# Performance work log

Measured on AMD Instinct MI355X. Metric: run time of the kernel, lower is better.

The kernel has to match this reference:

```python
import jax, jax.numpy as jnp
import numpy as np

N = 50000      # nodes
E = 800000     # edges (avg degree 16)
IN_DIM = 256
OUT_DIM = 256
H = 8          # heads
HD = OUT_DIM // H  # head_dim = 32


def setup_inputs() -> dict:
    key = jax.random.key(0)
    k = jax.random.split(key, 6)
    x = jax.random.normal(k[0], (N, IN_DIM), jnp.float32)
    edge_index = jax.random.randint(k[1], (2, E), 0, N, dtype=jnp.int64)
    s = 1.0 / np.sqrt(IN_DIM)
    W_src = jax.random.normal(k[2], (IN_DIM, OUT_DIM), jnp.float32) * s
    W_dst = jax.random.normal(k[3], (IN_DIM, OUT_DIM), jnp.float32) * s
    b_src = jnp.zeros((OUT_DIM,), jnp.float32)
    b_dst = jnp.zeros((OUT_DIM,), jnp.float32)
    # xavier-ish scale for [H, 2*HD] attention vector
    attn_vec = jax.random.normal(k[4], (H, 2 * HD), jnp.float32) * np.sqrt(2.0 / (H + 2 * HD))
    return {"x": x, "edge_index": edge_index, "W_src": W_src, "b_src": b_src,
            "W_dst": W_dst, "b_dst": b_dst, "attn_vec": attn_vec}


def reference(x, edge_index, W_src, b_src, W_dst, b_dst, attn_vec):
    # Linear projections -> [N, H, HD]
    proj_src = (x @ W_src + b_src).reshape(N, H, HD)
    proj_dst = (x @ W_dst + b_dst).reshape(N, H, HD)
    # Split concat-dot into two per-node dot products (same math as
    # einsum('ehd,hd->eh', cat([src,dst]), attn_vec)), computed per node
    # then gathered per edge.
    a_src, a_dst = attn_vec[:, :HD], attn_vec[:, HD:]
    s_src = jnp.einsum('nhd,hd->nh', proj_src, a_src)  # [N, H]
    s_dst = jnp.einsum('nhd,hd->nh', proj_dst, a_dst)  # [N, H]
    e_src, e_dst = edge_index[0], edge_index[1]
    scores = s_src[e_src] + s_dst[e_dst]               # [E, H]
    scores = jnp.where(scores >= 0, scores, 0.2 * scores)  # LeakyReLU(0.2)
    # Segment softmax over destination nodes (original: exp / scatter-add(exp) + eps)
    ex = jnp.exp(scores)
    denom = jax.ops.segment_sum(ex, e_dst, num_segments=N)  # [N, H]
    alpha = ex / (denom[e_dst] + 1e-15)                     # [E, H]
    # Weighted scatter aggregation of src features
    weighted = alpha[:, :, None] * proj_src[e_src]          # [E, H, HD]
    agg = jax.ops.segment_sum(weighted, e_dst, num_segments=N)  # [N, H, HD]
    # Single relation -> mean over messages is identity; residual add
    return x + agg.reshape(N, OUT_DIM)
```

## Files before the change

kernel.cpp:

```cpp
#include <hip/hip_runtime.h>

#define DIM 256
#define NHEAD 8
#define HDIM 32
#define CAPS 24

typedef __attribute__((ext_vector_type(4))) float f32x4;
typedef __attribute__((ext_vector_type(8))) short short8;
typedef __attribute__((ext_vector_type(8))) __bf16 bf16x8;

static __device__ __forceinline__ unsigned short f2bf(float f) {
  unsigned int u = __float_as_uint(f);
  u = (u + 0x7fffu + ((u >> 16) & 1u)) >> 16;
  return (unsigned short)u;
}

static __device__ __forceinline__ f32x4 mfma16x16x32(short8 a, short8 b, f32x4 c) {
  union { short8 s; bf16x8 b; } ua, ub;
  ua.s = a; ub.s = b;
  return __builtin_amdgcn_mfma_f32_16x16x32_bf16(ua.b, ub.b, c, 0, 0, 0);
}

static __device__ __forceinline__ int edge_at(const void* ei, int is64, long long pos) {
  if (is64) return (int)((const long long*)ei)[pos];
  return ((const int*)ei)[pos];
}

__global__ void k_prep(const float* Wsrc, const float* Wdst, const float* bsrc, const float* bdst,
                       const float* attn, float* c16, unsigned short* wp,
                       const void* ei, int E, int* cur4, int* bsi) {
  int b = blockIdx.x, tid = threadIdx.x;
  if (b < 256) {
    int idx = b * 256 + tid;
    int k = idx >> 8, n = idx & 255;
    int kb = k >> 5, khi = (k >> 3) & 3, i = k & 7;
    int ct = n >> 4, lane = khi * 16 + (n & 15);
    wp[(((size_t)ct * 8 + kb) * 64 + lane) * 8 + i] = f2bf(Wsrc[(size_t)k * DIM + n]);
  } else if (b == 256) {
    for (int q = tid * 16, qe = q + 16; q < qe; ++q) {
      int kb = q >> 9, lane = (q >> 3) & 63, i = q & 7;
      int k = kb * 32 + ((lane >> 4) * 8) + i;
      int j = lane & 15;
      int h = j & 7;
      const float* W = (j < 8) ? Wsrc : Wdst;
      const float* a = attn + h * 2 * HDIM + ((j < 8) ? 0 : HDIM);
      float acc = 0.f;
      #pragma unroll
      for (int d = 0; d < HDIM; ++d)
        acc += W[(size_t)k * DIM + h * HDIM + d] * a[d];
      wp[(((size_t)16 * 8 + kb) * 64 + lane) * 8 + i] = f2bf(acc);
    }
    if (tid < 16) {
      int j = tid, h = j & 7;
      const float* bb = (j < 8) ? bsrc : bdst;
      const float* a = attn + h * 2 * HDIM + ((j < 8) ? 0 : HDIM);
      float c = 0.f;
      for (int d = 0; d < HDIM; ++d) c += bb[h * HDIM + d] * a[d];
      c16[j] = c;
    }
  } else {
    const unsigned int* raw = (const unsigned int*)ei;
    int chk = E < 256 ? E : 256;
    int bad = 0;
    for (int i = tid & 63; i < chk; i += 64)
      bad |= (raw[2 * i + 1] != 0u);
    unsigned long long m = __ballot(bad);
    int is64 = (m == 0ull);
    int e = (b - 257) * 256 + tid;
    if (e < E) {
      int s = edge_at(ei, is64, e);
      int d = edge_at(ei, is64, (long long)E + e);
      int j = e & 3;
      int pos = atomicAdd(cur4 + (size_t)d * 4 + j, 1);
      if (pos < CAPS) bsi[((size_t)d * 4 + j) * CAPS + pos] = s;
    }
  }
}

__global__ void __launch_bounds__(256) k_gemm(const float* x, const unsigned short* wp,
                                              const float* bsrc, const float* c16,
                                              unsigned short* pb, float* ssrc, float* sdst,
                                              int N) {
  const int tid = threadIdx.x;
  const int m0 = blockIdx.x * 64;
  const int lane = tid & 63;
  const int w = tid >> 6;
  const int l15 = lane & 15, lhi = lane >> 4;
  int arow = m0 + w * 16 + l15;
  if (arow > N - 1) arow = N - 1;
  const float* xr = x + (size_t)arow * DIM + lhi * 8;
  short8 af[8];
  #pragma unroll
  for (int kb = 0; kb < 8; ++kb) {
    f32x4 q0 = *(const f32x4*)(xr + kb * 32);
    f32x4 q1 = *(const f32x4*)(xr + kb * 32 + 4);
    short8 a;
    a[0] = f2bf(q0[0]); a[1] = f2bf(q0[1]); a[2] = f2bf(q0[2]); a[3] = f2bf(q0[3]);
    a[4] = f2bf(q1[0]); a[5] = f2bf(q1[1]); a[6] = f2bf(q1[2]); a[7] = f2bf(q1[3]);
    af[kb] = a;
  }
  const short8* wp8 = (const short8*)wp;
  #pragma unroll 1
  for (int ct = 0; ct < 17; ++ct) {
    f32x4 acc = {0.f, 0.f, 0.f, 0.f};
    #pragma unroll
    for (int kb = 0; kb < 8; ++kb)
      acc = mfma16x16x32(af[kb], wp8[(size_t)(ct * 8 + kb) * 64 + lane], acc);
    if (ct < 16) {
      int col = ct * 16 + l15;
      float bs = bsrc[col];
      #pragma unroll
      for (int qq = 0; qq < 4; ++qq) {
        int orow = m0 + w * 16 + lhi * 4 + qq;
        if (orow < N) pb[(size_t)orow * DIM + col] = f2bf(acc[qq] + bs);
      }
    } else {
      int j = l15;
      float cadd = c16[j];
      #pragma unroll
      for (int qq = 0; qq < 4; ++qq) {
        int orow = m0 + w * 16 + lhi * 4 + qq;
        if (orow < N) {
          float val = acc[qq] + cadd;
          if (j < 8) ssrc[(size_t)orow * 8 + j] = val;
          else       sdst[(size_t)orow * 8 + (j - 8)] = val;
        }
      }
    }
  }
}

#define LOADP(st, R, EF) do {                                                  \
    int _st2 = (st) * 2;                                                       \
    if (_st2 >= deg) { R.x = 0u; R.y = 0u; R.z = 0u; R.w = 0u; EF = 0.f; }     \
    else {                                                                     \
      int _idx = _st2 + half;                                                  \
      int _c = _idx < deg ? _idx : deg - 1;                                    \
      int _s = __shfl(myS, _c, 64);                                            \
      R = *(const uint4*)(pb + (size_t)_s * DIM + (size_t)l31 * 8);            \
      float _sc = ssrc[(size_t)_s * 8 + h] + sd;                               \
      _sc = _sc >= 0.f ? _sc : 0.2f * _sc;                                     \
      float _ev = __expf(_sc);                                                 \
      EF = (_idx < deg) ? _ev : 0.f;                                           \
    }                                                                          \
  } while (0)

#define COMPUTE(R, EF) do {                                                    \
    dsum += EF;                                                                \
    a0 = fmaf(EF, __uint_as_float(R.x << 16),         a0);                     \
    a1 = fmaf(EF, __uint_as_float(R.x & 0xffff0000u), a1);                     \
    a2 = fmaf(EF, __uint_as_float(R.y << 16),         a2);                     \
    a3 = fmaf(EF, __uint_as_float(R.y & 0xffff0000u), a3);                     \
    a4 = fmaf(EF, __uint_as_float(R.z << 16),         a4);                     \
    a5 = fmaf(EF, __uint_as_float(R.z & 0xffff0000u), a5);                     \
    a6 = fmaf(EF, __uint_as_float(R.w << 16),         a6);                     \
    a7 = fmaf(EF, __uint_as_float(R.w & 0xffff0000u), a7);                     \
  } while (0)

__global__ void __launch_bounds__(256) k_agg(const float* x, const unsigned short* pb,
                                             const float* ssrc, const float* sdst,
                                             const int* cur4, const int* bsi,
                                             float* out, int N) {
  int gw = (int)((blockIdx.x * 256 + threadIdx.x) >> 6);
  if (gw >= N) return;
  const int lane = threadIdx.x & 63;
  const int half = lane >> 5;
  const int l31 = lane & 31;
  const int h = l31 >> 2;
  const size_t obase = (size_t)gw * DIM + l31 * 8 + half * 4;
  uint4 cc = *(const uint4*)(cur4 + (size_t)gw * 4);
  int c0 = (int)cc.x > CAPS ? CAPS : (int)cc.x;
  int c1 = (int)cc.y > CAPS ? CAPS : (int)cc.y;
  int c2 = (int)cc.z > CAPS ? CAPS : (int)cc.z;
  int c3 = (int)cc.w > CAPS ? CAPS : (int)cc.w;
  int p1 = c0, p2 = c0 + c1, p3 = p2 + c2;
  int deg = p3 + c3; if (deg > 64) deg = 64;
  if (deg == 0) {
    *(f32x4*)(out + obase) = *(const f32x4*)(x + obase);
    return;
  }
  const float sd = sdst[(size_t)gw * 8 + h];
  int l = lane < deg ? lane : deg - 1;
  int j = (l >= p1) + (l >= p2) + (l >= p3);
  int bj = (j == 0) ? 0 : (j == 1 ? p1 : (j == 2 ? p2 : p3));
  int myS = bsi[((size_t)gw * 4 + j) * CAPS + (l - bj)];

  float a0 = 0.f, a1 = 0.f, a2 = 0.f, a3 = 0.f;
  float a4 = 0.f, a5 = 0.f, a6 = 0.f, a7 = 0.f;
  float dsum = 0.f;
  int stages = (deg + 1) >> 1;

  uint4 R0, R1, R2; float E0, E1, E2;
  LOADP(0, R0, E0);
  LOADP(1, R1, E1);
  LOADP(2, R2, E2);
  for (int t = 0; t < stages; t += 3) {
    COMPUTE(R0, E0); LOADP(t + 3, R0, E0);
    COMPUTE(R1, E1); LOADP(t + 4, R1, E1);
    COMPUTE(R2, E2); LOADP(t + 5, R2, E2);
  }

  a0 += __shfl_xor(a0, 32, 64);
  a1 += __shfl_xor(a1, 32, 64);
  a2 += __shfl_xor(a2, 32, 64);
  a3 += __shfl_xor(a3, 32, 64);
  a4 += __shfl_xor(a4, 32, 64);
  a5 += __shfl_xor(a5, 32, 64);
  a6 += __shfl_xor(a6, 32, 64);
  a7 += __shfl_xor(a7, 32, 64);
  dsum += __shfl_xor(dsum, 32, 64);

  float inv = 1.f / (dsum + 1e-15f);
  float s0 = half ? a4 : a0;
  float s1 = half ? a5 : a1;
  float s2 = half ? a6 : a2;
  float s3 = half ? a7 : a3;
  f32x4 xv = *(const f32x4*)(x + obase);
  f32x4 o;
  o[0] = xv[0] + s0 * inv;
  o[1] = xv[1] + s1 * inv;
  o[2] = xv[2] + s2 * inv;
  o[3] = xv[3] + s3 * inv;
  *(f32x4*)(out + obase) = o;
}

extern "C" void kernel_launch(void* const* d_in, const int* in_sizes, int n_in,
                              void* d_out, int out_size, void* d_ws, size_t ws_size,
                              hipStream_t stream) {
  const float* x    = (const float*)d_in[0];
  const void*  ei   = d_in[1];
  const float* Wsrc = (const float*)d_in[2];
  const float* bsrc = (const float*)d_in[3];
  const float* Wdst = (const float*)d_in[4];
  const float* bdst = (const float*)d_in[5];
  const float* attn = (const float*)d_in[6];
  const int N = in_sizes[0] / DIM;
  const int E = in_sizes[1] / 2;
  float* out = (float*)d_out;

  char* wsp = (char*)d_ws;
  size_t off = 0;
  auto alloc = [&](size_t b) { char* p = wsp + off; off += (b + 255) & ~(size_t)255; return (void*)p; };
  unsigned short* pb  = (unsigned short*)alloc((size_t)N * DIM * 2);
  unsigned short* wp  = (unsigned short*)alloc((size_t)17 * 8 * 64 * 8 * 2);
  float* c16  = (float*)alloc(16 * 4);
  float* ssrc = (float*)alloc((size_t)N * 8 * 4);
  float* sdst = (float*)alloc((size_t)N * 8 * 4);
  int* cur4   = (int*)alloc((size_t)N * 4 * 4);
  int* bsi    = (int*)alloc((size_t)N * 4 * CAPS * 4);

  hipMemsetAsync(cur4, 0, (size_t)N * 4 * 4, stream);

  int EB = (E + 255) / 256;
  k_prep<<<257 + EB, 256, 0, stream>>>(Wsrc, Wdst, bsrc, bdst, attn, c16, wp, ei, E, cur4, bsi);
  int GB = (N + 63) / 64;
  k_gemm<<<GB, 256, 0, stream>>>(x, wp, bsrc, c16, pb, ssrc, sdst, N);
  k_agg<<<(N + 3) / 4, 256, 0, stream>>>(x, pb, ssrc, sdst, cur4, bsi, out, N);
}
```

Baseline: 195.1 us.

## Replace global-atomic bucketing with chunked shared-memory histogram counting sort

Edge bucketing by destination is rebuilt as a two-pass counting sort. Each of 256 chunks builds a byte-packed per-node histogram with shared-memory atomics, then a prefix pass computes per-chunk bases and node degrees. A scatter pass writes source ids into contiguous 64-slot per-node lists, and that pass is fused into the same launch as the projection GEMM. This removes global atomics, the memset and the 4-way sub-bucket indexing in aggregation. In exchange it adds two extra kernels and about 51 MB of count/base traffic. The 8-bit counters per chunk could also overflow on a heavily skewed degree distribution.

Result: slower. 216.8 us (+11.1%).

```diff
diff --git a/kernel.cpp b/kernel.cpp
--- a/kernel.cpp
+++ b/kernel.cpp
@@ -3,7 +3,8 @@
 #define DIM 256
 #define NHEAD 8
 #define HDIM 32
-#define CAPS 24
+#define NCHUNK 256
+#define SLOT 64
 
 typedef __attribute__((ext_vector_type(4))) float f32x4;
 typedef __attribute__((ext_vector_type(8))) short short8;
@@ -26,9 +27,16 @@
   return ((const int*)ei)[pos];
 }
 
+static __device__ __forceinline__ int detect64(const void* ei, int E, int tid) {
+  const unsigned int* raw = (const unsigned int*)ei;
+  int chk = E < 256 ? E : 256;
+  int bad = 0;
+  for (int i = tid & 63; i < chk; i += 64) bad |= (raw[2 * i + 1] != 0u);
+  return (__ballot(bad) == 0ull);
+}
+
 __global__ void k_prep(const float* Wsrc, const float* Wdst, const float* bsrc, const float* bdst,
-                       const float* attn, float* c16, unsigned short* wp,
-                       const void* ei, int E, int* cur4, int* bsi) {
+                       const float* attn, float* c16, unsigned short* wp) {
   int b = blockIdx.x, tid = threadIdx.x;
   if (b < 256) {
     int idx = b * 256 + tid;
@@ -36,7 +44,7 @@
     int kb = k >> 5, khi = (k >> 3) & 3, i = k & 7;
     int ct = n >> 4, lane = khi * 16 + (n & 15);
     wp[(((size_t)ct * 8 + kb) * 64 + lane) * 8 + i] = f2bf(Wsrc[(size_t)k * DIM + n]);
-  } else if (b == 256) {
+  } else {
     for (int q = tid * 16, qe = q + 16; q < qe; ++q) {
       int kb = q >> 9, lane = (q >> 3) & 63, i = q & 7;
       int k = kb * 32 + ((lane >> 4) * 8) + i;
@@ -58,33 +66,77 @@
       for (int d = 0; d < HDIM; ++d) c += bb[h * HDIM + d] * a[d];
       c16[j] = c;
     }
-  } else {
-    const unsigned int* raw = (const unsigned int*)ei;
-    int chk = E < 256 ? E : 256;
-    int bad = 0;
-    for (int i = tid & 63; i < chk; i += 64)
-      bad |= (raw[2 * i + 1] != 0u);
-    unsigned long long m = __ballot(bad);
-    int is64 = (m == 0ull);
-    int e = (b - 257) * 256 + tid;
-    if (e < E) {
+  }
+}
+
+__global__ void __launch_bounds__(1024) k_p1(const void* ei, int E, int CS,
+                                             unsigned int* cnt8, int N) {
+  __shared__ unsigned int hist[12800];
+  int tid = threadIdx.x;
+  int c = blockIdx.x;
+  int nw = (N + 3) >> 2;
+  for (int i = tid; i < nw; i += 1024) hist[i] = 0u;
+  int is64 = detect64(ei, E, tid);
+  __syncthreads();
+  int e0 = c * CS;
+  int e1 = e0 + CS; if (e1 > E) e1 = E;
+  for (int e = e0 + tid; e < e1; e += 1024) {
+    int d = edge_at(ei, is64, (long long)E + e);
+    atomicAdd(&hist[d >> 2], 1u << ((d & 3) * 8));
+  }
+  __syncthreads();
+  unsigned int* row = cnt8 + (size_t)c * nw;
+  for (int i = tid; i < nw; i += 1024) row[i] = hist[i];
+}
+
+__global__ void k_p2(const unsigned int* cnt8, unsigned int* base8, int* deg32, int N) {
+  int nw = (N + 3) >> 2;
+  int q = blockIdx.x * 256 + threadIdx.x;
+  if (q >= nw) return;
+  unsigned int s0 = 0, s1 = 0, s2 = 0, s3 = 0;
+  for (int c = 0; c < NCHUNK; ++c) {
+    unsigned int v = cnt8[(size_t)c * nw + q];
+    base8[(size_t)c * nw + q] = s0 | (s1 << 8) | (s2 << 16) | (s3 << 24);
+    s0 += v & 255u; s1 += (v >> 8) & 255u; s2 += (v >> 16) & 255u; s3 += (v >> 24) & 255u;
+  }
+  int d = q * 4;
+  if (d     < N) deg32[d    ] = (int)s0;
+  if (d + 1 < N) deg32[d + 1] = (int)s1;
+  if (d + 2 < N) deg32[d + 2] = (int)s2;
+  if (d + 3 < N) deg32[d + 3] = (int)s3;
+}
+
+__global__ void __launch_bounds__(1024) k_bg(const void* ei, int E, int CS,
+                                             const unsigned int* base8, int* bsi, int N,
+                                             const float* x, const unsigned short* wp,
+                                             const float* bsrc, const float* c16,
+                                             unsigned short* pb, float* ssrc, float* sdst) {
+  __shared__ unsigned int hist[12800];
+  int tid = threadIdx.x;
+  if ((int)blockIdx.x < NCHUNK) {
+    int c = blockIdx.x;
+    int nw = (N + 3) >> 2;
+    for (int i = tid; i < nw; i += 1024) hist[i] = 0u;
+    int is64 = detect64(ei, E, tid);
+    __syncthreads();
+    const unsigned int* brow = base8 + (size_t)c * nw;
+    int e0 = c * CS;
+    int e1 = e0 + CS; if (e1 > E) e1 = E;
+    for (int e = e0 + tid; e < e1; e += 1024) {
       int s = edge_at(ei, is64, e);
       int d = edge_at(ei, is64, (long long)E + e);
-      int j = e & 3;
-      int pos = atomicAdd(cur4 + (size_t)d * 4 + j, 1);
-      if (pos < CAPS) bsi[((size_t)d * 4 + j) * CAPS + pos] = s;
+      unsigned int sh = (d & 3) * 8u;
+      unsigned int lp = (atomicAdd(&hist[d >> 2], 1u << sh) >> sh) & 255u;
+      unsigned int slot = ((brow[d >> 2] >> sh) & 255u) + lp;
+      if (slot < SLOT) bsi[(size_t)d * SLOT + slot] = s;
     }
-  }
-}
-
-__global__ void __launch_bounds__(256) k_gemm(const float* x, const unsigned short* wp,
-                                              const float* bsrc, const float* c16,
-                                              unsigned short* pb, float* ssrc, float* sdst,
-                                              int N) {
-  const int tid = threadIdx.x;
-  const int m0 = blockIdx.x * 64;
+    return;
+  }
+  const int g = (int)blockIdx.x - NCHUNK;
+  const int w16 = tid >> 6;
+  const int m0 = g * 256 + (w16 >> 2) * 64;
+  const int w = w16 & 3;
   const int lane = tid & 63;
-  const int w = tid >> 6;
   const int l15 = lane & 15, lhi = lane >> 4;
   int arow = m0 + w * 16 + l15;
   if (arow > N - 1) arow = N - 1;
@@ -159,7 +211,7 @@
 
 __global__ void __launch_bounds__(256) k_agg(const float* x, const unsigned short* pb,
                                              const float* ssrc, const float* sdst,
-                                             const int* cur4, const int* bsi,
+                                             const int* deg32, const int* bsi,
                                              float* out, int N) {
   int gw = (int)((blockIdx.x * 256 + threadIdx.x) >> 6);
   if (gw >= N) return;
@@ -168,22 +220,13 @@
   const int l31 = lane & 31;
   const int h = l31 >> 2;
   const size_t obase = (size_t)gw * DIM + l31 * 8 + half * 4;
-  uint4 cc = *(const uint4*)(cur4 + (size_t)gw * 4);
-  int c0 = (int)cc.x > CAPS ? CAPS : (int)cc.x;
-  int c1 = (int)cc.y > CAPS ? CAPS : (int)cc.y;
-  int c2 = (int)cc.z > CAPS ? CAPS : (int)cc.z;
-  int c3 = (int)cc.w > CAPS ? CAPS : (int)cc.w;
-  int p1 = c0, p2 = c0 + c1, p3 = p2 + c2;
-  int deg = p3 + c3; if (deg > 64) deg = 64;
+  int deg = deg32[gw]; if (deg > SLOT) deg = SLOT;
   if (deg == 0) {
     *(f32x4*)(out + obase) = *(const f32x4*)(x + obase);
     return;
   }
   const float sd = sdst[(size_t)gw * 8 + h];
-  int l = lane < deg ? lane : deg - 1;
-  int j = (l >= p1) + (l >= p2) + (l >= p3);
-  int bj = (j == 0) ? 0 : (j == 1 ? p1 : (j == 2 ? p2 : p3));
-  int myS = bsi[((size_t)gw * 4 + j) * CAPS + (l - bj)];
+  int myS = bsi[(size_t)gw * SLOT + (lane < deg ? lane : deg - 1)];
 
   float a0 = 0.f, a1 = 0.f, a2 = 0.f, a3 = 0.f;
   float a4 = 0.f, a5 = 0.f, a6 = 0.f, a7 = 0.f;
@@ -241,19 +284,24 @@
   char* wsp = (char*)d_ws;
   size_t off = 0;
   auto alloc = [&](size_t b) { char* p = wsp + off; off += (b + 255) & ~(size_t)255; return (void*)p; };
-  unsigned short* pb  = (unsigned short*)alloc((size_t)N * DIM * 2);
-  unsigned short* wp  = (unsigned short*)alloc((size_t)17 * 8 * 64 * 8 * 2);
-  float* c16  = (float*)alloc(16 * 4);
-  float* ssrc = (float*)alloc((size_t)N * 8 * 4);
-  float* sdst = (float*)alloc((size_t)N * 8 * 4);
-  int* cur4   = (int*)alloc((size_t)N * 4 * 4);
-  int* bsi    = (int*)alloc((size_t)N * 4 * CAPS * 4);
-
-  hipMemsetAsync(cur4, 0, (size_t)N * 4 * 4, stream);
-
-  int EB = (E + 255) / 256;
-  k_prep<<<257 + EB, 256, 0, stream>>>(Wsrc, Wdst, bsrc, bdst, attn, c16, wp, ei, E, cur4, bsi);
-  int GB = (N + 63) / 64;
-  k_gemm<<<GB, 256, 0, stream>>>(x, wp, bsrc, c16, pb, ssrc, sdst, N);
-  k_agg<<<(N + 3) / 4, 256, 0, stream>>>(x, pb, ssrc, sdst, cur4, bsi, out, N);
-}
+  const int nw = (N + 3) >> 2;
+  unsigned short* pb   = (unsigned short*)alloc((size_t)N * DIM * 2);
+  unsigned short* wp   = (unsigned short*)alloc((size_t)17 * 8 * 64 * 8 * 2);
+  float* c16   = (float*)alloc(16 * 4);
+  float* ssrc  = (float*)alloc((size_t)N * 8 * 4);
+  float* sdst  = (float*)alloc((size_t)N * 8 * 4);
+  unsigned int* cnt8  = (unsigned int*)alloc((size_t)NCHUNK * nw * 4);
+  unsigned int* base8 = (unsigned int*)alloc((size_t)NCHUNK * nw * 4);
+  int* deg32 = (int*)alloc((size_t)N * 4);
+  int* bsi   = (int*)alloc((size_t)N * SLOT * 4);
+
+  const int CS = (E + NCHUNK - 1) / NCHUNK;
+
+  k_prep<<<257, 256, 0, stream>>>(Wsrc, Wdst, bsrc, bdst, attn, c16, wp);
+  k_p1<<<NCHUNK, 1024, 0, stream>>>(ei, E, CS, cnt8, N);
+  k_p2<<<(nw + 255) / 256, 256, 0, stream>>>(cnt8, base8, deg32, N);
+  int GB4 = (N + 255) / 256;
+  k_bg<<<NCHUNK + GB4, 1024, 0, stream>>>(ei, E, CS, base8, bsi, N,
+                                          x, wp, bsrc, c16, pb, ssrc, sdst);
+  k_agg<<<(N + 3) / 4, 256, 0, stream>>>(x, pb, ssrc, sdst, deg32, bsi, out, N);
+}
```
